# Kernel tuning notes

Hardware: AMD Instinct MI355X
Metric: run time of the kernel (lower is better)

Reference implementation:

```python
import jax, jax.numpy as jnp
import numpy as np

FD = 1024       # feature_dim
H = 16          # num_heads
D = FD // H     # head_dim = 64
SCALES = [64, 128, 256, 512, 1024]
S = len(SCALES) # num_scales = 5
LW = 3          # local_window
DEPTH = 8       # cantor_depth
B = 8192
C = 1000        # num_classes
GD = FD // 2    # gate hidden dim


def _cantor_coordinate(pos, max_len, depth):
    x = pos / max(1, max_len - 1)
    x = max(1e-06, min(x, 1.0 - 1e-06))
    val = 0.0
    factor = 0.5
    for _ in range(depth):
        x *= 3.0
        digit = int(x)
        x -= digit
        if digit == 2:
            val += factor
        factor *= 0.5
    return val


def _build_routes():
    coords = np.array([_cantor_coordinate(i, S, DEPTH) for i in range(S)], dtype=np.float32)
    routes = np.zeros((S, LW), dtype=np.int32)
    for i in range(S):
        d = np.abs(coords - coords[i])
        routes[i] = np.argsort(d, kind='stable')[:LW]
    return routes


def setup_inputs() -> dict:
    key = jax.random.key(0)
    ks = jax.random.split(key, 32)
    nrm = lambda k, shape, s=0.02: jax.random.normal(k, shape, jnp.float32) * s
    inp = {}
    inp['features'] = jax.random.normal(ks[0], (B, FD), jnp.float32)
    for i, sc in enumerate(SCALES):
        inp[f'sf_{i}'] = jax.random.normal(ks[1 + i], (B, sc), jnp.float32)
    for i in range(S):
        inp[f'logits_{i}'] = jax.random.normal(ks[6 + i], (B, C), jnp.float32)
    for i, sc in enumerate(SCALES):
        inp[f'Ws_{i}'] = nrm(ks[11 + i], (FD, sc))
    inp['bs'] = jnp.zeros((S, FD), jnp.float32)
    inp['scale_emb'] = nrm(ks[16], (S, FD))
    inp['Wq'] = nrm(ks[17], (FD, FD)); inp['bq'] = jnp.zeros((FD,), jnp.float32)
    inp['Wk'] = nrm(ks[18], (FD, FD)); inp['bk'] = jnp.zeros((FD,), jnp.float32)
    inp['Wv'] = nrm(ks[19], (FD, FD)); inp['bv'] = jnp.zeros((FD,), jnp.float32)
    inp['Wg1'] = nrm(ks[20], (GD, FD)); inp['bg1'] = jnp.zeros((GD,), jnp.float32)
    inp['g_gamma'] = jnp.ones((GD,), jnp.float32); inp['g_beta'] = jnp.zeros((GD,), jnp.float32)
    inp['Wg2'] = nrm(ks[21], (S, GD)); inp['bg2'] = jnp.zeros((S,), jnp.float32)
    inp['temperature'] = jnp.asarray(0.07, jnp.float32)
    inp['routes'] = jnp.asarray(_build_routes())
    return inp


def reference(features, sf_0, sf_1, sf_2, sf_3, sf_4,
              logits_0, logits_1, logits_2, logits_3, logits_4,
              Ws_0, Ws_1, Ws_2, Ws_3, Ws_4, bs, scale_emb,
              Wq, bq, Wk, bk, Wv, bv,
              Wg1, bg1, g_gamma, g_beta, Wg2, bg2,
              temperature, routes):
    sfs = [sf_0, sf_1, sf_2, sf_3, sf_4]
    Wss = [Ws_0, Ws_1, Ws_2, Ws_3, Ws_4]
    # per-scale projection to common dim + scale embedding -> [B, S, FD]
    common = jnp.stack([sfs[i] @ Wss[i].T + bs[i] + scale_emb[i] for i in range(S)], axis=1)
    Bn = features.shape[0]
    Q = (features @ Wq.T + bq).reshape(Bn, H, D)                       # [B,H,D] (seq len 1)
    K = (common @ Wk.T + bk).reshape(Bn, S, H, D).transpose(0, 2, 1, 3)  # [B,H,S,D]
    V = (common @ Wv.T + bv).reshape(Bn, S, H, D).transpose(0, 2, 1, 3)  # [B,H,S,D]
    # Cantor-routed gather over scale axis: [B,H,S,LW,D]
    k_g = K[:, :, routes, :]
    v_g = V[:, :, routes, :]
    scores = jnp.einsum('bhd,bhswd->bhsw', Q, k_g) / jnp.sqrt(jnp.asarray(D, jnp.float32))
    attn = jax.nn.softmax(scores / jnp.abs(temperature), axis=-1)
    out = jnp.einsum('bhsw,bhswd->bhsd', attn, v_g)                    # [B,H,S,D]
    scale_importance = jnp.linalg.norm(out, axis=-1).mean(axis=1)      # [B,S]
    # gate net: Linear -> LayerNorm -> GELU(exact) -> Linear (dropout off in eval)
    h = features @ Wg1.T + bg1
    mu = h.mean(axis=-1, keepdims=True)
    var = h.var(axis=-1, keepdims=True)
    h = (h - mu) / jnp.sqrt(var + 1e-5) * g_gamma + g_beta
    h = jax.nn.gelu(h, approximate=False)
    gate_logits = h @ Wg2.T + bg2                                      # [B,S]
    alpha = 0.7
    combined_scores = alpha * scale_importance + (1 - alpha) * gate_logits
    attention_weights = jax.nn.softmax(combined_scores, axis=-1)       # [B,S]
    logits_stack = jnp.stack([logits_0, logits_1, logits_2, logits_3, logits_4], axis=1)  # [B,S,C]
    combined_logits = jnp.einsum('bs,bsc->bc', attention_weights, logits_stack)
    return (combined_logits, attention_weights)
```

## Files before the change

kernel.cpp:

```cpp
#include <hip/hip_runtime.h>


typedef short s16x8 __attribute__((ext_vector_type(8)));
typedef ushort u16x8 __attribute__((ext_vector_type(8)));
typedef float f32x4 __attribute__((ext_vector_type(4)));

__device__ __forceinline__ ushort f2b(float x) {
  unsigned u = __float_as_uint(x);
  return (ushort)((u + 0x7fffu + ((u >> 16) & 1u)) >> 16);
}
__device__ __forceinline__ float b2f(ushort u) {
  return __uint_as_float(((unsigned)u) << 16);
}

struct GemmJob {
  const ushort* X; const ushort* W; ushort* C; const float* bias;
  int ldx, ldw, ldo, K, N, pad;
};
struct GemmJobs { GemmJob j[6]; };

__global__ __launch_bounds__(256, 2) void mega_gemm(GemmJobs jobs)
{
  __shared__ __align__(16) ushort smem[2][128 * 64];
  ushort* As = smem[0];
  ushort* Bs = smem[1];
  const GemmJob jb = jobs.j[blockIdx.z];
  const int bn = blockIdx.y << 7;
  if (bn >= jb.N) return;
  const int bm = blockIdx.x << 7;
  const int tid = threadIdx.x;
  const int wave = tid >> 6, lane = tid & 63;
  const int wm = (wave >> 1) << 6, wn = (wave & 1) << 6;
  const int quad = lane >> 4, l16 = lane & 15;

  f32x4 acc[4][4];
  const f32x4 zero = {0.f, 0.f, 0.f, 0.f};
#pragma unroll
  for (int i = 0; i < 4; ++i)
#pragma unroll
    for (int j = 0; j < 4; ++j) acc[i][j] = zero;

  const int ktiles = jb.K >> 6;
  for (int kt = 0; kt < ktiles; ++kt) {
    const int kbase = kt << 6;
    __syncthreads();
#pragma unroll
    for (int i = 0; i < 4; ++i) {
      int wb = (i << 8) + (wave << 6);
      int flat = wb + lane;
      int row = flat >> 3, slot = flat & 7;
      int c = slot ^ (row & 7);
      const ushort* src = jb.X + (size_t)(bm + row) * jb.ldx + kbase + (c << 3);
      __builtin_amdgcn_global_load_lds(
          (const __attribute__((address_space(1))) void*)src,
          (__attribute__((address_space(3))) void*)(As + ((size_t)wb << 3)),
          16, 0, 0);
    }
#pragma unroll
    for (int i = 0; i < 4; ++i) {
      int wb = (i << 8) + (wave << 6);
      int flat = wb + lane;
      int row = flat >> 3, slot = flat & 7;
      int c = slot ^ (row & 7);
      const ushort* src = jb.W + (size_t)(bn + row) * jb.ldw + kbase + (c << 3);
      __builtin_amdgcn_global_load_lds(
          (const __attribute__((address_space(1))) void*)src,
          (__attribute__((address_space(3))) void*)(Bs + ((size_t)wb << 3)),
          16, 0, 0);
    }
    __syncthreads();
#pragma unroll
    for (int k0 = 0; k0 < 2; ++k0) {
      s16x8 af[4], bfr[4];
#pragma unroll
      for (int t = 0; t < 4; ++t) {
        int row = wm + (t << 4) + l16;
        int slot = ((k0 << 2) + quad) ^ (row & 7);
        af[t] = *(const s16x8*)(As + ((row << 3) + slot) * 8);
      }
#pragma unroll
      for (int t = 0; t < 4; ++t) {
        int row = wn + (t << 4) + l16;
        int slot = ((k0 << 2) + quad) ^ (row & 7);
        bfr[t] = *(const s16x8*)(Bs + ((row << 3) + slot) * 8);
      }
#pragma unroll
      for (int i = 0; i < 4; ++i)
#pragma unroll
        for (int j = 0; j < 4; ++j)
          acc[i][j] = __builtin_amdgcn_mfma_f32_16x16x32_bf16(af[i], bfr[j], acc[i][j], 0, 0, 0);
    }
  }

  __syncthreads();
  ushort* Cs = (ushort*)smem;
#pragma unroll
  for (int j = 0; j < 4; ++j) {
    float bv = jb.bias[bn + wn + (j << 4) + l16];
#pragma unroll
    for (int i = 0; i < 4; ++i) {
      int row = wm + (i << 4) + (quad << 2);
      int col = wn + (j << 4) + l16;
#pragma unroll
      for (int r = 0; r < 4; ++r)
        Cs[(row + r) * 128 + col] = f2b(acc[i][j][r] + bv);
    }
  }
  __syncthreads();
#pragma unroll
  for (int p = 0; p < 8; ++p) {
    int chunk = (p << 8) + tid;
    int row = chunk >> 4, c8 = chunk & 15;
    int4 v = *(const int4*)(Cs + row * 128 + (c8 << 3));
    *(int4*)(jb.C + (size_t)(bm + row) * jb.ldo + bn + (c8 << 3)) = v;
  }
}

__global__ __launch_bounds__(256, 2) void gemm_xwt(
    const ushort* __restrict__ X, int ldx, const ushort* __restrict__ W, int ldw,
    ushort* __restrict__ Cv, int ldo, int M, int N, int K)
{
  __shared__ __align__(16) ushort As[128 * 64];
  __shared__ __align__(16) ushort Bs[128 * 64];
  const int tid = threadIdx.x;
  const int bm = blockIdx.x << 7, bn = blockIdx.y << 7;
  const int wave = tid >> 6, lane = tid & 63;
  const int wm = (wave >> 1) << 6, wn = (wave & 1) << 6;
  const int quad = lane >> 4, l16 = lane & 15;

  f32x4 acc[4][4];
  const f32x4 zero = {0.f, 0.f, 0.f, 0.f};
#pragma unroll
  for (int i = 0; i < 4; ++i)
#pragma unroll
    for (int j = 0; j < 4; ++j) acc[i][j] = zero;

  const int ktiles = K >> 6;
  for (int kt = 0; kt < ktiles; ++kt) {
    const int kbase = kt << 6;
    __syncthreads();
#pragma unroll
    for (int i = 0; i < 4; ++i) {
      int wb = (i << 8) + (wave << 6);
      int flat = wb + lane;
      int row = flat >> 3, slot = flat & 7;
      int c = slot ^ (row & 7);
      int gr = bm + row; gr = (gr < M) ? gr : (M - 1);
      const ushort* src = X + (size_t)gr * ldx + kbase + (c << 3);
      __builtin_amdgcn_global_load_lds(
          (const __attribute__((address_space(1))) void*)src,
          (__attribute__((address_space(3))) void*)(As + ((size_t)wb << 3)),
          16, 0, 0);
    }
#pragma unroll
    for (int i = 0; i < 4; ++i) {
      int wb = (i << 8) + (wave << 6);
      int flat = wb + lane;
      int row = flat >> 3, slot = flat & 7;
      int c = slot ^ (row & 7);
      int gr = bn + row; gr = (gr < N) ? gr : (N - 1);
      const ushort* src = W + (size_t)gr * ldw + kbase + (c << 3);
      __builtin_amdgcn_global_load_lds(
          (const __attribute__((address_space(1))) void*)src,
          (__attribute__((address_space(3))) void*)(Bs + ((size_t)wb << 3)),
          16, 0, 0);
    }
    __syncthreads();
#pragma unroll
    for (int k0 = 0; k0 < 2; ++k0) {
      s16x8 af[4], bfr[4];
#pragma unroll
      for (int t = 0; t < 4; ++t) {
        int row = wm + (t << 4) + l16;
        int slot = ((k0 << 2) + quad) ^ (row & 7);
        af[t] = *(const s16x8*)(As + ((row << 3) + slot) * 8);
      }
#pragma unroll
      for (int t = 0; t < 4; ++t) {
        int row = wn + (t << 4) + l16;
        int slot = ((k0 << 2) + quad) ^ (row & 7);
        bfr[t] = *(const s16x8*)(Bs + ((row << 3) + slot) * 8);
      }
#pragma unroll
      for (int i = 0; i < 4; ++i)
#pragma unroll
        for (int j = 0; j < 4; ++j)
          acc[i][j] = __builtin_amdgcn_mfma_f32_16x16x32_bf16(af[i], bfr[j], acc[i][j], 0, 0, 0);
    }
  }
#pragma unroll
  for (int j = 0; j < 4; ++j) {
    int gn = bn + wn + (j << 4) + l16;
    if (gn < N) {
#pragma unroll
      for (int i = 0; i < 4; ++i) {
#pragma unroll
        for (int r = 0; r < 4; ++r) {
          int gm = bm + wm + (i << 4) + (quad << 2) + r;
          if (gm < M) ((ushort*)Cv)[(size_t)gm * ldo + gn] = f2b(acc[i][j][r]);
        }
      }
    }
  }
}

__global__ __launch_bounds__(256) void ckv_kernel(
    const ushort* __restrict__ bse, const ushort* __restrict__ Wkvb,
    const float* __restrict__ bkv, float* __restrict__ ckv)
{
  int w = (blockIdx.x << 2) + (threadIdx.x >> 6);
  int lane = threadIdx.x & 63;
  int s = w >> 11, n = w & 2047;
  const ushort* a = bse + s * 1024 + (lane << 4);
  const ushort* b = Wkvb + (size_t)n * 1024 + (lane << 4);
  u16x8 a0 = ((const u16x8*)a)[0], a1 = ((const u16x8*)a)[1];
  u16x8 b0 = ((const u16x8*)b)[0], b1 = ((const u16x8*)b)[1];
  float sum = 0.f;
#pragma unroll
  for (int t = 0; t < 8; ++t)
    sum += b2f(a0[t]) * b2f(b0[t]) + b2f(a1[t]) * b2f(b1[t]);
#pragma unroll
  for (int m = 1; m < 64; m <<= 1) sum += __shfl_xor(sum, m, 64);
  if (lane == 0) ckv[s * 2048 + n] = sum + bkv[n];
}

__device__ __forceinline__ void cvt4(const float* __restrict__ s, int si_,
                                     ushort* __restrict__ d, int di) {
  float4 v = ((const float4*)s)[si_];
  ushort4 o; o.x = f2b(v.x); o.y = f2b(v.y); o.z = f2b(v.z); o.w = f2b(v.w);
  ((ushort4*)d)[di] = o;
}

__global__ __launch_bounds__(256) void prep_all(
    const float* __restrict__ feat,
    const float* __restrict__ s0, const float* __restrict__ s1,
    const float* __restrict__ s2, const float* __restrict__ s3,
    const float* __restrict__ s4,
    const float* __restrict__ Wq, const float* __restrict__ Wg1,
    const float* __restrict__ Wk, const float* __restrict__ Wv,
    const float* __restrict__ bs, const float* __restrict__ semb,
    const float* __restrict__ bk, const float* __restrict__ bv,
    const float* __restrict__ bq, const float* __restrict__ bg1,
    const float* __restrict__ Ws0, const float* __restrict__ Ws1,
    const float* __restrict__ Ws2, const float* __restrict__ Ws3,
    const float* __restrict__ Ws4,
    ushort* __restrict__ featb, ushort* __restrict__ sfc,
    ushort* __restrict__ Wqh, ushort* __restrict__ Wkvb,
    ushort* __restrict__ bse, float* __restrict__ bkv,
    float* __restrict__ bqg1, ushort* __restrict__ WsT)
{
  __shared__ float tile[64][65];
  int bx = blockIdx.x, t = threadIdx.x;
  if (bx < 8192) {
    int b = bx;
    {
      float4 v = ((const float4*)(feat + (size_t)b * 1024))[t];
      ushort4 o; o.x = f2b(v.x); o.y = f2b(v.y); o.z = f2b(v.z); o.w = f2b(v.w);
      ((ushort4*)(featb + (size_t)b * 1024))[t] = o;
    }
    for (int c = t; c < 496; c += 256) {
      int e = c << 2;
      const float* src;
      if (e < 64)        src = s0 + (size_t)b * 64 + e;
      else if (e < 192)  src = s1 + (size_t)b * 128 + (e - 64);
      else if (e < 448)  src = s2 + (size_t)b * 256 + (e - 192);
      else if (e < 960)  src = s3 + (size_t)b * 512 + (e - 448);
      else               src = s4 + (size_t)b * 1024 + (e - 960);
      float4 v = *(const float4*)src;
      ushort4 o; o.x = f2b(v.x); o.y = f2b(v.y); o.z = f2b(v.z); o.w = f2b(v.w);
      ((ushort4*)(sfc + (size_t)b * 1984))[c] = o;
    }
    return;
  }
  if (bx < 11785) {
    int id = (bx - 8192) * 256 + t;
    if (id < 262144) { cvt4(Wq, id, Wqh, id); return; }
    id -= 262144;
    if (id < 131072) { cvt4(Wg1, id, Wqh + 1048576, id); return; }
    id -= 131072;
    if (id < 262144) { cvt4(Wk, id, Wkvb, id); return; }
    id -= 262144;
    if (id < 262144) { cvt4(Wv, id, Wkvb + 1048576, id); return; }
    id -= 262144;
    if (id < 1280) {
      float4 a = ((const float4*)bs)[id];
      float4 b = ((const float4*)semb)[id];
      ushort4 o; o.x = f2b(a.x + b.x); o.y = f2b(a.y + b.y);
      o.z = f2b(a.z + b.z); o.w = f2b(a.w + b.w);
      ((ushort4*)bse)[id] = o;
      return;
    }
    id -= 1280;
    if (id < 512) {
      float4 v = (id < 256) ? ((const float4*)bk)[id] : ((const float4*)bv)[id - 256];
      ((float4*)bkv)[id] = v;
      return;
    }
    id -= 512;
    if (id < 384) {
      float4 v = (id < 256) ? ((const float4*)bq)[id] : ((const float4*)bg1)[id - 256];
      ((float4*)bqg1)[id] = v;
    }
    return;
  }
  {
    int f = bx - 11785;
    int kt = f % 31, ct = f / 31;
    const float* Ws; int kb, scj, offj;
    if (kt < 1)       { Ws = Ws0; kb = kt;      scj = 64;   offj = 0;   }
    else if (kt < 3)  { Ws = Ws1; kb = kt - 1;  scj = 128;  offj = 64;  }
    else if (kt < 7)  { Ws = Ws2; kb = kt - 3;  scj = 256;  offj = 192; }
    else if (kt < 15) { Ws = Ws3; kb = kt - 7;  scj = 512;  offj = 448; }
    else              { Ws = Ws4; kb = kt - 15; scj = 1024; offj = 960; }
    int c0 = ct << 6, k0 = kb << 6;
    int col = t & 63, r4 = t >> 6;
#pragma unroll
    for (int p = 0; p < 16; ++p) {
      int r = (p << 2) + r4;
      tile[r][col] = Ws[(size_t)(c0 + r) * scj + k0 + col];
    }
    __syncthreads();
#pragma unroll
    for (int p = 0; p < 16; ++p) {
      int r = (p << 2) + r4;
      WsT[(size_t)(offj + k0 + r) * 1024 + c0 + col] = f2b(tile[col][r]);
    }
  }
}

__global__ __launch_bounds__(256) void attn_gate_kernel(
    const ushort* __restrict__ QH, const ushort* __restrict__ KV,
    const int* __restrict__ routes, const float* __restrict__ temp,
    const float* __restrict__ g_gamma, const float* __restrict__ g_beta,
    const float* __restrict__ Wg2, const float* __restrict__ bg2,
    float* __restrict__ aw)
{
  const int wave = threadIdx.x >> 6, lane = threadIdx.x & 63;
  const int b = (blockIdx.x << 2) + wave;
  const ushort* q = QH + (size_t)b * 1536 + (lane << 4);
  const ushort* kv = KV + (size_t)b * 10240 + (lane << 4);

  float qv[16];
  {
    u16x8 q0 = ((const u16x8*)q)[0];
    u16x8 q1 = ((const u16x8*)q)[1];
#pragma unroll
    for (int t = 0; t < 8; ++t) { qv[t] = b2f(q0[t]); qv[8 + t] = b2f(q1[t]); }
  }
  float vv[5][16];
  float p[20];
#pragma unroll
  for (int j = 0; j < 5; ++j) {
    u16x8 k0 = ((const u16x8*)(kv + j * 2048))[0];
    u16x8 k1 = ((const u16x8*)(kv + j * 2048))[1];
    u16x8 v0 = ((const u16x8*)(kv + j * 2048 + 1024))[0];
    u16x8 v1 = ((const u16x8*)(kv + j * 2048 + 1024))[1];
    float s = 0.f;
#pragma unroll
    for (int t = 0; t < 8; ++t) {
      s += qv[t] * b2f(k0[t]) + qv[8 + t] * b2f(k1[t]);
      vv[j][t] = b2f(v0[t]); vv[j][8 + t] = b2f(v1[t]);
    }
    p[j] = s;
  }
  {
    int idx = 5;
#pragma unroll
    for (int a = 0; a < 5; ++a)
#pragma unroll
      for (int c2 = a; c2 < 5; ++c2) {
        float s = 0.f;
#pragma unroll
        for (int t = 0; t < 16; ++t) s += vv[a][t] * vv[c2][t];
        p[idx++] = s;
      }
  }
#pragma unroll
  for (int t = 0; t < 20; ++t) {
    p[t] += __shfl_xor(p[t], 1, 64);
    p[t] += __shfl_xor(p[t], 2, 64);
  }
  float inv = 1.0f / (8.0f * fabsf(temp[0]));
  float si5[5];
#pragma unroll
  for (int s = 0; s < 5; ++s) {
    int r0 = routes[s * 3 + 0], r1 = routes[s * 3 + 1], r2 = routes[s * 3 + 2];
    float x0 = p[r0] * inv, x1 = p[r1] * inv, x2 = p[r2] * inv;
    float mx = fmaxf(x0, fmaxf(x1, x2));
    float e0 = __expf(x0 - mx), e1 = __expf(x1 - mx), e2 = __expf(x2 - mx);
    float den = e0 + e1 + e2;
    float a0 = e0 / den, a1 = e1 / den, a2 = e2 / den;
    auto G = [&](int i, int j2) -> float {
      int a = i < j2 ? i : j2, bb = i < j2 ? j2 : i;
      return p[5 + 5 * a - ((a * (a - 1)) >> 1) + (bb - a)];
    };
    float val = a0 * a0 * G(r0, r0) + a1 * a1 * G(r1, r1) + a2 * a2 * G(r2, r2)
              + 2.f * (a0 * a1 * G(r0, r1) + a0 * a2 * G(r0, r2) + a1 * a2 * G(r1, r2));
    float o = sqrtf(fmaxf(val, 0.f));
    o += __shfl_xor(o, 4, 64);  o += __shfl_xor(o, 8, 64);
    o += __shfl_xor(o, 16, 64); o += __shfl_xor(o, 32, 64);
    si5[s] = o * (1.f / 16.f);
  }

  const ushort* hr = QH + (size_t)b * 1536 + 1024 + (lane << 3);
  float hv[8], s1 = 0.f, s2 = 0.f;
  {
    u16x8 h8 = *(const u16x8*)hr;
#pragma unroll
    for (int t = 0; t < 8; ++t) {
      float x = b2f(h8[t]);
      hv[t] = x; s1 += x; s2 += x * x;
    }
  }
#pragma unroll
  for (int m = 1; m < 64; m <<= 1) {
    s1 += __shfl_xor(s1, m, 64);
    s2 += __shfl_xor(s2, m, 64);
  }
  float mean = s1 * (1.f / 512.f);
  float var = s2 * (1.f / 512.f) - mean * mean;
  float rstd = rsqrtf(var + 1e-5f);
  float4 gg0 = ((const float4*)(g_gamma + (lane << 3)))[0];
  float4 gg1 = ((const float4*)(g_gamma + (lane << 3)))[1];
  float4 gb0 = ((const float4*)(g_beta + (lane << 3)))[0];
  float4 gb1 = ((const float4*)(g_beta + (lane << 3)))[1];
  float gam[8] = {gg0.x, gg0.y, gg0.z, gg0.w, gg1.x, gg1.y, gg1.z, gg1.w};
  float bet[8] = {gb0.x, gb0.y, gb0.z, gb0.w, gb1.x, gb1.y, gb1.z, gb1.w};
  float gel[8];
#pragma unroll
  for (int t = 0; t < 8; ++t) {
    float x = (hv[t] - mean) * rstd * gam[t] + bet[t];
    gel[t] = 0.5f * x * (1.f + erff(x * 0.70710678118654752f));
  }
  float acc5[5];
#pragma unroll
  for (int s = 0; s < 5; ++s) {
    const float* wr = Wg2 + s * 512 + (lane << 3);
    float4 w0 = ((const float4*)wr)[0];
    float4 w1 = ((const float4*)wr)[1];
    float a = gel[0] * w0.x + gel[1] * w0.y + gel[2] * w0.z + gel[3] * w0.w
            + gel[4] * w1.x + gel[5] * w1.y + gel[6] * w1.z + gel[7] * w1.w;
#pragma unroll
    for (int m = 1; m < 64; m <<= 1) a += __shfl_xor(a, m, 64);
    acc5[s] = a;
  }
  if (lane == 0) {
    float cs[5];
#pragma unroll
    for (int s = 0; s < 5; ++s)
      cs[s] = 0.7f * si5[s] + 0.3f * (acc5[s] + bg2[s]);
    float mx = cs[0];
#pragma unroll
    for (int s = 1; s < 5; ++s) mx = fmaxf(mx, cs[s]);
    float e[5], sum = 0.f;
#pragma unroll
    for (int s = 0; s < 5; ++s) { e[s] = __expf(cs[s] - mx); sum += e[s]; }
    float rs = 1.f / sum;
#pragma unroll
    for (int s = 0; s < 5; ++s) aw[(size_t)b * 5 + s] = e[s] * rs;
  }
}

__global__ __launch_bounds__(256) void combine_kernel(
    const float* __restrict__ aw,
    const float* __restrict__ l0, const float* __restrict__ l1,
    const float* __restrict__ l2, const float* __restrict__ l3,
    const float* __restrict__ l4, float* __restrict__ out)
{
  int b = blockIdx.x, t = threadIdx.x;
  float a0 = aw[(size_t)b * 5 + 0], a1 = aw[(size_t)b * 5 + 1],
        a2 = aw[(size_t)b * 5 + 2], a3 = aw[(size_t)b * 5 + 3],
        a4 = aw[(size_t)b * 5 + 4];
  if (t < 250) {
    size_t base = (size_t)b * 250 + t;
    float4 x0 = ((const float4*)l0)[base];
    float4 x1 = ((const float4*)l1)[base];
    float4 x2 = ((const float4*)l2)[base];
    float4 x3 = ((const float4*)l3)[base];
    float4 x4 = ((const float4*)l4)[base];
    float4 r;
    r.x = a0 * x0.x + a1 * x1.x + a2 * x2.x + a3 * x3.x + a4 * x4.x;
    r.y = a0 * x0.y + a1 * x1.y + a2 * x2.y + a3 * x3.y + a4 * x4.y;
    r.z = a0 * x0.z + a1 * x1.z + a2 * x2.z + a3 * x3.z + a4 * x4.z;
    r.w = a0 * x0.w + a1 * x1.w + a2 * x2.w + a3 * x3.w + a4 * x4.w;
    ((float4*)out)[base] = r;
  }
}

extern "C" void kernel_launch(void* const* d_in, const int* in_sizes, int n_in,
                              void* d_out, int out_size, void* d_ws, size_t ws_size,
                              hipStream_t stream) {
  const float* features = (const float*)d_in[0];
  const float* sf0 = (const float*)d_in[1];
  const float* sf1 = (const float*)d_in[2];
  const float* sf2 = (const float*)d_in[3];
  const float* sf3 = (const float*)d_in[4];
  const float* sf4 = (const float*)d_in[5];
  const float* lg0 = (const float*)d_in[6];
  const float* lg1 = (const float*)d_in[7];
  const float* lg2 = (const float*)d_in[8];
  const float* lg3 = (const float*)d_in[9];
  const float* lg4 = (const float*)d_in[10];
  const float* Ws0 = (const float*)d_in[11];
  const float* Ws1 = (const float*)d_in[12];
  const float* Ws2 = (const float*)d_in[13];
  const float* Ws3 = (const float*)d_in[14];
  const float* Ws4 = (const float*)d_in[15];
  const float* bs   = (const float*)d_in[16];
  const float* semb = (const float*)d_in[17];
  const float* Wq  = (const float*)d_in[18];
  const float* bq  = (const float*)d_in[19];
  const float* Wk  = (const float*)d_in[20];
  const float* bk  = (const float*)d_in[21];
  const float* Wv  = (const float*)d_in[22];
  const float* bv  = (const float*)d_in[23];
  const float* Wg1 = (const float*)d_in[24];
  const float* bg1 = (const float*)d_in[25];
  const float* g_gamma = (const float*)d_in[26];
  const float* g_beta  = (const float*)d_in[27];
  const float* Wg2 = (const float*)d_in[28];
  const float* bg2 = (const float*)d_in[29];
  const float* temp = (const float*)d_in[30];
  const int* routes = (const int*)d_in[31];

  char* w = (char*)d_ws;
  ushort* sfc   = (ushort*)w;                 w += 8192ull * 1984 * 2;
  ushort* featb = (ushort*)w;                 w += 8192ull * 1024 * 2;
  ushort* Wqh   = (ushort*)w;                 w += 1536ull * 1024 * 2;
  ushort* WsT   = (ushort*)w;                 w += 1984ull * 1024 * 2;
  ushort* Akv   = (ushort*)w;                 w += 2048ull * 1984 * 2;
  ushort* Wkvb  = (ushort*)w;                 w += 2048ull * 1024 * 2;
  ushort* bse   = (ushort*)w;                 w += 5ull * 1024 * 2 + 256 - (5ull*1024*2)%256;
  float*  bkv   = (float*)w;                  w += 2048ull * 4;
  float*  bqg1  = (float*)w;                  w += 1536ull * 4;
  float*  ckv   = (float*)w;                  w += 5ull * 2048 * 4;
  float*  si_unused = (float*)w;              w += 8192ull * 5 * 4;
  ushort* QH    = (ushort*)w;                 w += 8192ull * 1536 * 2;
  ushort* KV    = (ushort*)w;                 w += 8192ull * 10240 * 2;
  (void)si_unused;

  float* out = (float*)d_out;
  float* aw = out + 8192ull * 1000;

  static const int offj[5] = {0, 64, 192, 448, 960};
  static const int scj[5]  = {64, 128, 256, 512, 1024};

  prep_all<<<12281, 256, 0, stream>>>(
      features, sf0, sf1, sf2, sf3, sf4,
      Wq, Wg1, Wk, Wv, bs, semb, bk, bv, bq, bg1,
      Ws0, Ws1, Ws2, Ws3, Ws4,
      featb, sfc, Wqh, Wkvb, bse, bkv, bqg1, WsT);

  gemm_xwt<<<dim3(16, 16), 256, 0, stream>>>(Wkvb, 1024, WsT, 1024,
                                             Akv, 1984, 2048, 1984, 1024);
  ckv_kernel<<<2560, 256, 0, stream>>>(bse, Wkvb, bkv, ckv);

  GemmJobs jobs;
  for (int j = 0; j < 5; ++j) {
    jobs.j[j].X = sfc + offj[j];  jobs.j[j].ldx = 1984;
    jobs.j[j].W = Akv + offj[j];  jobs.j[j].ldw = 1984;
    jobs.j[j].C = KV + j * 2048;  jobs.j[j].ldo = 10240;
    jobs.j[j].bias = ckv + (size_t)j * 2048;
    jobs.j[j].K = scj[j];  jobs.j[j].N = 2048;  jobs.j[j].pad = 0;
  }
  jobs.j[5].X = featb;  jobs.j[5].ldx = 1024;
  jobs.j[5].W = Wqh;    jobs.j[5].ldw = 1024;
  jobs.j[5].C = QH;     jobs.j[5].ldo = 1536;
  jobs.j[5].bias = bqg1;
  jobs.j[5].K = 1024;   jobs.j[5].N = 1536;  jobs.j[5].pad = 0;
  mega_gemm<<<dim3(64, 16, 6), 256, 0, stream>>>(jobs);

  attn_gate_kernel<<<2048, 256, 0, stream>>>(QH, KV, routes, temp,
                                             g_gamma, g_beta, Wg2, bg2, aw);
  combine_kernel<<<8192, 256, 0, stream>>>(aw, lg0, lg1, lg2, lg3, lg4, out);

  (void)in_sizes; (void)n_in; (void)out_size; (void)ws_size;
}
```

Baseline: 479.9 us.

## Fuse ckv into Akv GEMM, fuse combine into attention, pad C tile

Three changes. The bias-dot ckv kernel now runs as extra blocks inside the Akv GEMM launch, and the logits combine step runs inside the attention/gate kernel using per-block shared attention weights, which removes two kernel launches and the round trip of aw through global memory. The mega_gemm epilogue staging buffer gets a row pitch of 132 instead of 128 to reduce LDS bank conflicts, at the cost of more shared memory per block. The fused attention kernel now also streams five logits tensors, which may raise register or latency pressure in that kernel.

```diff
diff --git a/kernel.cpp b/kernel.cpp
--- a/kernel.cpp
+++ b/kernel.cpp
@@ -21,9 +21,9 @@
 
 __global__ __launch_bounds__(256, 2) void mega_gemm(GemmJobs jobs)
 {
-  __shared__ __align__(16) ushort smem[2][128 * 64];
-  ushort* As = smem[0];
-  ushort* Bs = smem[1];
+  __shared__ __align__(16) ushort smem[16896];
+  ushort* As = smem;
+  ushort* Bs = smem + 8192;
   const GemmJob jb = jobs.j[blockIdx.z];
   const int bn = blockIdx.y << 7;
   if (bn >= jb.N) return;
@@ -93,7 +93,7 @@
   }
 
   __syncthreads();
-  ushort* Cs = (ushort*)smem;
+  ushort* Cs = smem;
 #pragma unroll
   for (int j = 0; j < 4; ++j) {
     float bv = jb.bias[bn + wn + (j << 4) + l16];
@@ -103,7 +103,7 @@
       int col = wn + (j << 4) + l16;
 #pragma unroll
       for (int r = 0; r < 4; ++r)
-        Cs[(row + r) * 128 + col] = f2b(acc[i][j][r] + bv);
+        Cs[(row + r) * 132 + col] = f2b(acc[i][j][r] + bv);
     }
   }
   __syncthreads();
@@ -111,20 +111,43 @@
   for (int p = 0; p < 8; ++p) {
     int chunk = (p << 8) + tid;
     int row = chunk >> 4, c8 = chunk & 15;
-    int4 v = *(const int4*)(Cs + row * 128 + (c8 << 3));
+    int4 v = *(const int4*)(Cs + row * 132 + (c8 << 3));
     *(int4*)(jb.C + (size_t)(bm + row) * jb.ldo + bn + (c8 << 3)) = v;
   }
 }
 
-__global__ __launch_bounds__(256, 2) void gemm_xwt(
-    const ushort* __restrict__ X, int ldx, const ushort* __restrict__ W, int ldw,
-    ushort* __restrict__ Cv, int ldo, int M, int N, int K)
+__global__ __launch_bounds__(256, 2) void akv_ckv(
+    const ushort* __restrict__ Wkvb, const ushort* __restrict__ WsT,
+    ushort* __restrict__ Akv,
+    const ushort* __restrict__ bse, const float* __restrict__ bkv,
+    float* __restrict__ ckv)
 {
   __shared__ __align__(16) ushort As[128 * 64];
   __shared__ __align__(16) ushort Bs[128 * 64];
+  const int bx = blockIdx.x;
   const int tid = threadIdx.x;
-  const int bm = blockIdx.x << 7, bn = blockIdx.y << 7;
   const int wave = tid >> 6, lane = tid & 63;
+
+  if (bx >= 256) {
+    int w = ((bx - 256) << 2) + wave;
+    int s = w >> 11, n = w & 2047;
+    const ushort* a = bse + s * 1024 + (lane << 4);
+    const ushort* b = Wkvb + (size_t)n * 1024 + (lane << 4);
+    u16x8 a0 = ((const u16x8*)a)[0], a1 = ((const u16x8*)a)[1];
+    u16x8 b0 = ((const u16x8*)b)[0], b1 = ((const u16x8*)b)[1];
+    float sum = 0.f;
+#pragma unroll
+    for (int t = 0; t < 8; ++t)
+      sum += b2f(a0[t]) * b2f(b0[t]) + b2f(a1[t]) * b2f(b1[t]);
+#pragma unroll
+    for (int m = 1; m < 64; m <<= 1) sum += __shfl_xor(sum, m, 64);
+    if (lane == 0) ckv[s * 2048 + n] = sum + bkv[n];
+    return;
+  }
+
+  const int bm = (bx >> 4) << 7, bnn = (bx & 15) << 7;
+  const int M = 2048, N = 1984, K = 1024;
+  const int ldx = 1024, ldw = 1024, ldo = 1984;
   const int wm = (wave >> 1) << 6, wn = (wave & 1) << 6;
   const int quad = lane >> 4, l16 = lane & 15;
 
@@ -146,7 +169,7 @@
       int row = flat >> 3, slot = flat & 7;
       int c = slot ^ (row & 7);
       int gr = bm + row; gr = (gr < M) ? gr : (M - 1);
-      const ushort* src = X + (size_t)gr * ldx + kbase + (c << 3);
+      const ushort* src = Wkvb + (size_t)gr * ldx + kbase + (c << 3);
       __builtin_amdgcn_global_load_lds(
           (const __attribute__((address_space(1))) void*)src,
           (__attribute__((address_space(3))) void*)(As + ((size_t)wb << 3)),
@@ -158,8 +181,8 @@
       int flat = wb + lane;
       int row = flat >> 3, slot = flat & 7;
       int c = slot ^ (row & 7);
-      int gr = bn + row; gr = (gr < N) ? gr : (N - 1);
-      const ushort* src = W + (size_t)gr * ldw + kbase + (c << 3);
+      int gr = bnn + row; gr = (gr < N) ? gr : (N - 1);
+      const ushort* src = WsT + (size_t)gr * ldw + kbase + (c << 3);
       __builtin_amdgcn_global_load_lds(
           (const __attribute__((address_space(1))) void*)src,
           (__attribute__((address_space(3))) void*)(Bs + ((size_t)wb << 3)),
@@ -190,38 +213,18 @@
   }
 #pragma unroll
   for (int j = 0; j < 4; ++j) {
-    int gn = bn + wn + (j << 4) + l16;
+    int gn = bnn + wn + (j << 4) + l16;
     if (gn < N) {
 #pragma unroll
       for (int i = 0; i < 4; ++i) {
 #pragma unroll
         for (int r = 0; r < 4; ++r) {
           int gm = bm + wm + (i << 4) + (quad << 2) + r;
-          if (gm < M) ((ushort*)Cv)[(size_t)gm * ldo + gn] = f2b(acc[i][j][r]);
+          Akv[(size_t)gm * ldo + gn] = f2b(acc[i][j][r]);
         }
       }
     }
   }
-}
-
-__global__ __launch_bounds__(256) void ckv_kernel(
-    const ushort* __restrict__ bse, const ushort* __restrict__ Wkvb,
-    const float* __restrict__ bkv, float* __restrict__ ckv)
-{
-  int w = (blockIdx.x << 2) + (threadIdx.x >> 6);
-  int lane = threadIdx.x & 63;
-  int s = w >> 11, n = w & 2047;
-  const ushort* a = bse + s * 1024 + (lane << 4);
-  const ushort* b = Wkvb + (size_t)n * 1024 + (lane << 4);
-  u16x8 a0 = ((const u16x8*)a)[0], a1 = ((const u16x8*)a)[1];
-  u16x8 b0 = ((const u16x8*)b)[0], b1 = ((const u16x8*)b)[1];
-  float sum = 0.f;
-#pragma unroll
-  for (int t = 0; t < 8; ++t)
-    sum += b2f(a0[t]) * b2f(b0[t]) + b2f(a1[t]) * b2f(b1[t]);
-#pragma unroll
-  for (int m = 1; m < 64; m <<= 1) sum += __shfl_xor(sum, m, 64);
-  if (lane == 0) ckv[s * 2048 + n] = sum + bkv[n];
 }
 
 __device__ __forceinline__ void cvt4(const float* __restrict__ s, int si_,
@@ -328,13 +331,17 @@
   }
 }
 
-__global__ __launch_bounds__(256) void attn_gate_kernel(
+__global__ __launch_bounds__(256) void attn_gate_combine(
     const ushort* __restrict__ QH, const ushort* __restrict__ KV,
     const int* __restrict__ routes, const float* __restrict__ temp,
     const float* __restrict__ g_gamma, const float* __restrict__ g_beta,
     const float* __restrict__ Wg2, const float* __restrict__ bg2,
-    float* __restrict__ aw)
+    const float* __restrict__ l0, const float* __restrict__ l1,
+    const float* __restrict__ l2, const float* __restrict__ l3,
+    const float* __restrict__ l4,
+    float* __restrict__ aw, float* __restrict__ out)
 {
+  __shared__ float awsh[4][5];
   const int wave = threadIdx.x >> 6, lane = threadIdx.x & 63;
   const int b = (blockIdx.x << 2) + wave;
   const ushort* q = QH + (size_t)b * 1536 + (lane << 4);
@@ -457,33 +464,34 @@
     for (int s = 0; s < 5; ++s) { e[s] = __expf(cs[s] - mx); sum += e[s]; }
     float rs = 1.f / sum;
 #pragma unroll
-    for (int s = 0; s < 5; ++s) aw[(size_t)b * 5 + s] = e[s] * rs;
-  }
-}
-
-__global__ __launch_bounds__(256) void combine_kernel(
-    const float* __restrict__ aw,
-    const float* __restrict__ l0, const float* __restrict__ l1,
-    const float* __restrict__ l2, const float* __restrict__ l3,
-    const float* __restrict__ l4, float* __restrict__ out)
-{
-  int b = blockIdx.x, t = threadIdx.x;
-  float a0 = aw[(size_t)b * 5 + 0], a1 = aw[(size_t)b * 5 + 1],
-        a2 = aw[(size_t)b * 5 + 2], a3 = aw[(size_t)b * 5 + 3],
-        a4 = aw[(size_t)b * 5 + 4];
+    for (int s = 0; s < 5; ++s) {
+      float v = e[s] * rs;
+      aw[(size_t)b * 5 + s] = v;
+      awsh[wave][s] = v;
+    }
+  }
+  __syncthreads();
+
+  const int t = threadIdx.x;
   if (t < 250) {
-    size_t base = (size_t)b * 250 + t;
-    float4 x0 = ((const float4*)l0)[base];
-    float4 x1 = ((const float4*)l1)[base];
-    float4 x2 = ((const float4*)l2)[base];
-    float4 x3 = ((const float4*)l3)[base];
-    float4 x4 = ((const float4*)l4)[base];
-    float4 r;
-    r.x = a0 * x0.x + a1 * x1.x + a2 * x2.x + a3 * x3.x + a4 * x4.x;
-    r.y = a0 * x0.y + a1 * x1.y + a2 * x2.y + a3 * x3.y + a4 * x4.y;
-    r.z = a0 * x0.z + a1 * x1.z + a2 * x2.z + a3 * x3.z + a4 * x4.z;
-    r.w = a0 * x0.w + a1 * x1.w + a2 * x2.w + a3 * x3.w + a4 * x4.w;
-    ((float4*)out)[base] = r;
+#pragma unroll
+    for (int r = 0; r < 4; ++r) {
+      int row = (blockIdx.x << 2) + r;
+      float a0 = awsh[r][0], a1 = awsh[r][1], a2 = awsh[r][2],
+            a3 = awsh[r][3], a4 = awsh[r][4];
+      size_t base = (size_t)row * 250 + t;
+      float4 x0 = ((const float4*)l0)[base];
+      float4 x1 = ((const float4*)l1)[base];
+      float4 x2 = ((const float4*)l2)[base];
+      float4 x3 = ((const float4*)l3)[base];
+      float4 x4 = ((const float4*)l4)[base];
+      float4 rr;
+      rr.x = a0 * x0.x + a1 * x1.x + a2 * x2.x + a3 * x3.x + a4 * x4.x;
+      rr.y = a0 * x0.y + a1 * x1.y + a2 * x2.y + a3 * x3.y + a4 * x4.y;
+      rr.z = a0 * x0.z + a1 * x1.z + a2 * x2.z + a3 * x3.z + a4 * x4.z;
+      rr.w = a0 * x0.w + a1 * x1.w + a2 * x2.w + a3 * x3.w + a4 * x4.w;
+      ((float4*)out)[base] = rr;
+    }
   }
 }
 
@@ -534,10 +542,8 @@
   float*  bkv   = (float*)w;                  w += 2048ull * 4;
   float*  bqg1  = (float*)w;                  w += 1536ull * 4;
   float*  ckv   = (float*)w;                  w += 5ull * 2048 * 4;
-  float*  si_unused = (float*)w;              w += 8192ull * 5 * 4;
   ushort* QH    = (ushort*)w;                 w += 8192ull * 1536 * 2;
   ushort* KV    = (ushort*)w;                 w += 8192ull * 10240 * 2;
-  (void)si_unused;
 
   float* out = (float*)d_out;
   float* aw = out + 8192ull * 1000;
@@ -551,9 +557,7 @@
       Ws0, Ws1, Ws2, Ws3, Ws4,
       featb, sfc, Wqh, Wkvb, bse, bkv, bqg1, WsT);
 
-  gemm_xwt<<<dim3(16, 16), 256, 0, stream>>>(Wkvb, 1024, WsT, 1024,
-                                             Akv, 1984, 2048, 1984, 1024);
-  ckv_kernel<<<2560, 256, 0, stream>>>(bse, Wkvb, bkv, ckv);
+  akv_ckv<<<2816, 256, 0, stream>>>(Wkvb, WsT, Akv, bse, bkv, ckv);
 
   GemmJobs jobs;
   for (int j = 0; j < 5; ++j) {
@@ -570,9 +574,10 @@
   jobs.j[5].K = 1024;   jobs.j[5].N = 1536;  jobs.j[5].pad = 0;
   mega_gemm<<<dim3(64, 16, 6), 256, 0, stream>>>(jobs);
 
-  attn_gate_kernel<<<2048, 256, 0, stream>>>(QH, KV, routes, temp,
-                                             g_gamma, g_beta, Wg2, bg2, aw);
-  combine_kernel<<<8192, 256, 0, stream>>>(aw, lg0, lg1, lg2, lg3, lg4, out);
+  attn_gate_combine<<<2048, 256, 0, stream>>>(QH, KV, routes, temp,
+                                              g_gamma, g_beta, Wg2, bg2,
+                                              lg0, lg1, lg2, lg3, lg4,
+                                              aw, out);
 
   (void)in_sizes; (void)n_in; (void)out_size; (void)ws_size;
 }
```

Measured after the change: 484.4 us. Within noise of the previous version (+0.9%).
